# Optimization experiments

Hardware: AMD Instinct MI355X
Metric: run time of the kernel (lower is better)

## Reference

```python
import jax, jax.numpy as jnp
import numpy as np

N = 8192       # tokens (batch*seq)
D = 4096       # input_size / d_model
H = 256        # gate hidden_size
E = 64         # num_experts
K = 2          # top_k


def setup_inputs() -> dict:
    key = jax.random.key(0)
    k0, k1, k2, k3 = jax.random.split(key, 4)
    x = jax.random.normal(k0, (N, D), dtype=jnp.float32)
    # nn.Linear default init: U(-1/sqrt(fan_in), 1/sqrt(fan_in))
    w1 = jax.random.uniform(k1, (H, D), jnp.float32, -1.0, 1.0) / np.sqrt(D)
    b1 = jax.random.uniform(k2, (H,), jnp.float32, -1.0, 1.0) / np.sqrt(D)
    w2 = jax.random.uniform(k3, (E, H), jnp.float32, -1.0, 1.0) / np.sqrt(H)
    return {"x": x, "w1": w1, "b1": b1, "w2": w2}


def reference(x, w1, b1, w2):
    # MLP gate: Linear -> GELU (exact erf, torch default) -> Dropout(eval: identity) -> Linear(no bias)
    h = jax.nn.gelu(jnp.einsum('nd,hd->nh', x, w1) + b1, approximate=False)  # [N, H]
    logits = jnp.einsum('nh,eh->ne', h, w2)                                  # [N, E]
    probs = jax.nn.softmax(logits, axis=-1)                                  # [N, E]
    # deterministic top-k path (sample_topk=0 / eval mode)
    top_k_gates, top_k_indices = jax.lax.top_k(probs, K)                     # [N, K] each
    return top_k_indices, top_k_gates, probs
```

## Files before the change

kernel.cpp:

```cpp
#include <hip/hip_runtime.h>
#include <hip/hip_bf16.h>
#include <math.h>

#define NTOK 8192
#define DIN  4096
#define HG   256
#define NE   64
#define SPLITK 4
#define KSTEPS 32
#define TR   16

typedef __attribute__((ext_vector_type(8))) short short8;
typedef __attribute__((ext_vector_type(4))) short short4v;
typedef __attribute__((ext_vector_type(4))) float f32x4;

__device__ __forceinline__ unsigned short f2bf_rne(float f) {
    union { float f; unsigned int u; } v; v.f = f;
    unsigned int r = v.u + 0x7fffu + ((v.u >> 16) & 1u);
    return (unsigned short)(r >> 16);
}
__device__ __forceinline__ float bf2f(unsigned short b) {
    union { unsigned int u; float f; } v; v.u = ((unsigned int)b) << 16;
    return v.f;
}

typedef const __attribute__((address_space(1))) unsigned int* gptr_t;
typedef __attribute__((address_space(3))) unsigned int* lptr_t;
__device__ __forceinline__ void gload_lds16(const void* g, void* l) {
    __builtin_amdgcn_global_load_lds((gptr_t)g, (lptr_t)l, 16, 0, 0);
}

__global__ __launch_bounds__(512) void convert_w1_kernel(
    const float* __restrict__ w1, unsigned short* __restrict__ w1t)
{
    const int id    = blockIdx.x * 512 + threadIdx.x;
    const int lane  = id & 63;
    const int cg    = id >> 6;
    const int kstep = cg >> 5;
    const int c     = cg & 31;
    const int hl    = c >> 4;
    const int unit  = c & 15;
    const int n     = unit * 16 + (lane & 15);
    const int k     = kstep * 32 + ((lane >> 4) & 3) * 8;

    const float* src = w1 + (size_t)n * DIN + k;
    short8 v;
#pragma unroll
    for (int j = 0; j < 8; ++j) {
        float f = src[j];
        unsigned short hi = f2bf_rne(f);
        v[j] = (hl == 0) ? (short)hi : (short)f2bf_rne(f - bf2f(hi));
    }
    *(short8*)(w1t + (size_t)cg * 512 + lane * 8) = v;
}

__global__ __launch_bounds__(512, 4) void gemm1_mfma_kernel(
    const float* __restrict__ x, const unsigned short* __restrict__ w1t,
    float* __restrict__ P)
{
    __shared__ unsigned short As[2][4][512];
    __shared__ unsigned short Bs[2][2][16][512];

    const int bid  = blockIdx.x;
    const int mblk = bid & 127;
    const int s    = bid >> 7;
    const int t    = threadIdx.x;
    const int lane = t & 63;
    const int w    = t >> 6;
    const int wm   = w >> 2;
    const int wn   = w & 3;

    const int m_base = mblk * 64;
    const int kstep0 = s * KSTEPS;

    const int a_unit = t >> 7;
    const int a_slot = (t >> 1) & 63;
    const int a_half = t & 1;
    const int a_row  = a_unit * 16 + (a_slot & 15);
    const int a_koff = (a_slot >> 4) * 8 + a_half * 4;
    const float* asrc = x + (size_t)(m_base + a_row) * DIN
                          + (size_t)kstep0 * 32 + a_koff;
    const int a_ldso = a_slot * 8 + a_half * 4;

    f32x4 acc[2][4];
#pragma unroll
    for (int i = 0; i < 2; ++i)
#pragma unroll
        for (int j = 0; j < 4; ++j) acc[i][j] = (f32x4)0.f;

#define CVT4_STORE(F)                                                         \
    {   short4v vh_, vl_;                                                     \
        float ff_[4] = { (F).x, (F).y, (F).z, (F).w };                        \
        _Pragma("unroll")                                                     \
        for (int j_ = 0; j_ < 4; ++j_) {                                      \
            unsigned short h_ = f2bf_rne(ff_[j_]);                            \
            vh_[j_] = (short)h_;                                              \
            vl_[j_] = (short)f2bf_rne(ff_[j_] - bf2f(h_));                    \
        }                                                                     \
        *(short4v*)&As[0][a_unit][a_ldso] = vh_;                              \
        *(short4v*)&As[1][a_unit][a_ldso] = vl_;                              \
    }

#pragma unroll
    for (int i = 0; i < 4; ++i) {
        const int c = w * 4 + i;
        gload_lds16(w1t + ((size_t)kstep0 * 32 + c) * 512 + lane * 8,
                    &Bs[0][c >> 4][c & 15][0]);
    }
    {
        float4 a0 = *(const float4*)(asrc);
        CVT4_STORE(a0)
    }
    __syncthreads();

#pragma unroll 1
    for (int tt = 0; tt < KSTEPS; ++tt) {
        const int bcur = tt & 1, bnxt = bcur ^ 1;
        const bool last = (tt == KSTEPS - 1);

        float4 nx;
        if (!last) {
            nx = *(const float4*)(asrc + (size_t)(tt + 1) * 32);
#pragma unroll
            for (int i = 0; i < 4; ++i) {
                const int c = w * 4 + i;
                gload_lds16(w1t + ((size_t)(kstep0 + tt + 1) * 32 + c) * 512 + lane * 8,
                            &Bs[bnxt][c >> 4][c & 15][0]);
            }
        }

        short8 ahf[2], alf[2], bhf[4], blf[4];
#pragma unroll
        for (int mr = 0; mr < 2; ++mr) {
            ahf[mr] = *(const short8*)&As[0][wm * 2 + mr][lane * 8];
            alf[mr] = *(const short8*)&As[1][wm * 2 + mr][lane * 8];
        }
#pragma unroll
        for (int nr = 0; nr < 4; ++nr) {
            bhf[nr] = *(const short8*)&Bs[bcur][0][wn * 4 + nr][lane * 8];
            blf[nr] = *(const short8*)&Bs[bcur][1][wn * 4 + nr][lane * 8];
        }

#pragma unroll
        for (int mr = 0; mr < 2; ++mr)
#pragma unroll
            for (int nr = 0; nr < 4; ++nr)
                acc[mr][nr] = __builtin_amdgcn_mfma_f32_16x16x32_bf16(
                    ahf[mr], bhf[nr], acc[mr][nr], 0, 0, 0);
#pragma unroll
        for (int mr = 0; mr < 2; ++mr)
#pragma unroll
            for (int nr = 0; nr < 4; ++nr)
                acc[mr][nr] = __builtin_amdgcn_mfma_f32_16x16x32_bf16(
                    ahf[mr], blf[nr], acc[mr][nr], 0, 0, 0);
#pragma unroll
        for (int mr = 0; mr < 2; ++mr)
#pragma unroll
            for (int nr = 0; nr < 4; ++nr)
                acc[mr][nr] = __builtin_amdgcn_mfma_f32_16x16x32_bf16(
                    alf[mr], bhf[nr], acc[mr][nr], 0, 0, 0);

        if (!last) {
            __syncthreads();
            CVT4_STORE(nx)
            __syncthreads();
        }
    }
#undef CVT4_STORE

    float* pb = P + (size_t)s * ((size_t)NTOK * HG);
#pragma unroll
    for (int mr = 0; mr < 2; ++mr)
#pragma unroll
        for (int nr = 0; nr < 4; ++nr) {
            const int n = wn * 64 + nr * 16 + (lane & 15);
#pragma unroll
            for (int r = 0; r < 4; ++r) {
                const int m = m_base + wm * 32 + mr * 16 + ((lane >> 4) & 3) * 4 + r;
                pb[(size_t)m * HG + n] = acc[mr][nr][r];
            }
        }
}

__global__ __launch_bounds__(512, 4) void reduce_gate_kernel(
    const float* __restrict__ P, const float* __restrict__ b1,
    const float* __restrict__ w2, float* __restrict__ out)
{
    __shared__ float h_lds[TR][260];
    __shared__ float lg[NE][33];

    const int t    = threadIdx.x;
    const int lane = t & 63;
    const int w    = t >> 6;
    const int r0   = blockIdx.x * TR;
    const size_t SS = (size_t)NTOK * HG;

    {
        const int row = t >> 5;
        const int sg  = t & 31;
        const size_t base = (size_t)(r0 + row) * HG + sg * 8;

        float q[8];
#pragma unroll
        for (int half = 0; half < 2; ++half) {
            float4 v0 = *(const float4*)(P + base + half * 4);
            float4 v1 = *(const float4*)(P + base + SS + half * 4);
            float4 v2 = *(const float4*)(P + base + 2 * SS + half * 4);
            float4 v3 = *(const float4*)(P + base + 3 * SS + half * 4);
            float4 bb = *(const float4*)(b1 + sg * 8 + half * 4);
            q[half * 4 + 0] = v0.x + v1.x + v2.x + v3.x + bb.x;
            q[half * 4 + 1] = v0.y + v1.y + v2.y + v3.y + bb.y;
            q[half * 4 + 2] = v0.z + v1.z + v2.z + v3.z + bb.z;
            q[half * 4 + 3] = v0.w + v1.w + v2.w + v3.w + bb.w;
        }
#pragma unroll
        for (int c = 0; c < 8; ++c)
            q[c] = 0.5f * q[c] * (1.0f + erff(q[c] * 0.70710678118654752440f));

        *(float4*)&h_lds[row][sg * 8]     = make_float4(q[0], q[1], q[2], q[3]);
        *(float4*)&h_lds[row][sg * 8 + 4] = make_float4(q[4], q[5], q[6], q[7]);
    }
    __syncthreads();

    const int e0   = w * 8;
    const int rowp = lane & 15;
    const int kq   = lane >> 4;

    float acc[8];
#pragma unroll
    for (int i = 0; i < 8; ++i) acc[i] = 0.f;

    const float* w2b = w2 + (size_t)e0 * HG + kq * 64;
#pragma unroll 1
    for (int kc = 0; kc < 64; kc += 8) {
        float a[8];
        *(float4*)&a[0] = *(const float4*)&h_lds[rowp][kq * 64 + kc];
        *(float4*)&a[4] = *(const float4*)&h_lds[rowp][kq * 64 + kc + 4];
#pragma unroll
        for (int n = 0; n < 8; ++n) {
            const float* wr = w2b + (size_t)n * HG + kc;
            float4 w0 = *(const float4*)(wr);
            float4 w1v = *(const float4*)(wr + 4);
            acc[n] = fmaf(w0.x, a[0], acc[n]);
            acc[n] = fmaf(w0.y, a[1], acc[n]);
            acc[n] = fmaf(w0.z, a[2], acc[n]);
            acc[n] = fmaf(w0.w, a[3], acc[n]);
            acc[n] = fmaf(w1v.x, a[4], acc[n]);
            acc[n] = fmaf(w1v.y, a[5], acc[n]);
            acc[n] = fmaf(w1v.z, a[6], acc[n]);
            acc[n] = fmaf(w1v.w, a[7], acc[n]);
        }
    }
#pragma unroll
    for (int n = 0; n < 8; ++n) {
        acc[n] += __shfl_xor(acc[n], 16);
        acc[n] += __shfl_xor(acc[n], 32);
    }
    if (lane < 16) {
#pragma unroll
        for (int n = 0; n < 8; ++n) lg[e0 + n][rowp] = acc[n];
    }
    __syncthreads();

    if (t < TR) {
        float l[NE];
#pragma unroll
        for (int e = 0; e < NE; ++e) l[e] = lg[e][t];

        float mx = l[0];
#pragma unroll
        for (int e = 1; e < NE; ++e) mx = fmaxf(mx, l[e]);

        float ssum = 0.f;
#pragma unroll
        for (int e = 0; e < NE; ++e) { float p = expf(l[e] - mx); l[e] = p; ssum += p; }
        const float inv = 1.0f / ssum;
#pragma unroll
        for (int e = 0; e < NE; ++e) l[e] *= inv;

        float v1 = -1.0f, v2 = -2.0f;
        int   i1 = 0,     i2 = 0;
#pragma unroll
        for (int e = 0; e < NE; ++e) {
            const float p  = l[e];
            const bool  g1 = p > v1;
            const bool  g2 = p > v2;
            const float nv2 = g1 ? v1 : (g2 ? p : v2);
            const int   ni2 = g1 ? i1 : (g2 ? e : i2);
            v1 = g1 ? p : v1;
            i1 = g1 ? e : i1;
            v2 = nv2;
            i2 = ni2;
        }

        const int row = r0 + t;
        float* out_idx  = out;
        float* out_gate = out + 2 * NTOK;
        float* out_prob = out + 4 * NTOK;
        out_idx[2 * row + 0]  = (float)i1;
        out_idx[2 * row + 1]  = (float)i2;
        out_gate[2 * row + 0] = v1;
        out_gate[2 * row + 1] = v2;

        float* pr = out_prob + (size_t)row * NE;
#pragma unroll
        for (int e = 0; e < NE; e += 4)
            *(float4*)(pr + e) = make_float4(l[e], l[e + 1], l[e + 2], l[e + 3]);
    }
}

extern "C" void kernel_launch(void* const* d_in, const int* in_sizes, int n_in,
                              void* d_out, int out_size, void* d_ws, size_t ws_size,
                              hipStream_t stream) {
    const float* x  = (const float*)d_in[0];
    const float* w1 = (const float*)d_in[1];
    const float* b1 = (const float*)d_in[2];
    const float* w2 = (const float*)d_in[3];
    float* out = (float*)d_out;

    unsigned short* w1t = (unsigned short*)d_ws;
    float* P = (float*)((char*)d_ws + (4u << 20));

    convert_w1_kernel<<<512, 512, 0, stream>>>(w1, w1t);
    gemm1_mfma_kernel<<<512, 512, 0, stream>>>(x, w1t, P);
    reduce_gate_kernel<<<512, 512, 0, stream>>>(P, b1, w2, out);
}
```

Measured before the change: 91.14 us.

## Use 4-wave blocks with 64x64 warp tiles and double-buffered A in LDS

The GEMM1 kernel moves from 8 waves to 4 waves per block, so each wave computes a 64x64 output tile (4x4 MFMA tiles) instead of 32x64. This raises register reuse of the A and B fragments and cuts LDS reads per MFMA. The converted A tile is now double-buffered in LDS, which removes one of the two barriers per k-step. In exchange each wave holds more accumulator registers and fewer waves are resident to hide latency.

```diff
diff --git a/kernel.cpp b/kernel.cpp
--- a/kernel.cpp
+++ b/kernel.cpp
@@ -54,11 +54,11 @@
     *(short8*)(w1t + (size_t)cg * 512 + lane * 8) = v;
 }
 
-__global__ __launch_bounds__(512, 4) void gemm1_mfma_kernel(
+__global__ __launch_bounds__(256, 2) void gemm1_mfma_kernel(
     const float* __restrict__ x, const unsigned short* __restrict__ w1t,
     float* __restrict__ P)
 {
-    __shared__ unsigned short As[2][4][512];
+    __shared__ unsigned short As[2][2][4][512];
     __shared__ unsigned short Bs[2][2][16][512];
 
     const int bid  = blockIdx.x;
@@ -67,49 +67,48 @@
     const int t    = threadIdx.x;
     const int lane = t & 63;
     const int w    = t >> 6;
-    const int wm   = w >> 2;
-    const int wn   = w & 3;
 
     const int m_base = mblk * 64;
     const int kstep0 = s * KSTEPS;
 
-    const int a_unit = t >> 7;
-    const int a_slot = (t >> 1) & 63;
-    const int a_half = t & 1;
-    const int a_row  = a_unit * 16 + (a_slot & 15);
-    const int a_koff = (a_slot >> 4) * 8 + a_half * 4;
+    const int a_unit = t >> 6;
+    const int a_q    = t & 63;
+    const int a_row  = a_unit * 16 + (a_q & 15);
+    const int a_koff = (a_q >> 4) * 8;
     const float* asrc = x + (size_t)(m_base + a_row) * DIN
                           + (size_t)kstep0 * 32 + a_koff;
-    const int a_ldso = a_slot * 8 + a_half * 4;
-
-    f32x4 acc[2][4];
-#pragma unroll
-    for (int i = 0; i < 2; ++i)
+    const int a_ldso = a_q * 8;
+
+    f32x4 acc[4][4];
+#pragma unroll
+    for (int i = 0; i < 4; ++i)
 #pragma unroll
         for (int j = 0; j < 4; ++j) acc[i][j] = (f32x4)0.f;
 
-#define CVT4_STORE(F)                                                         \
-    {   short4v vh_, vl_;                                                     \
-        float ff_[4] = { (F).x, (F).y, (F).z, (F).w };                        \
+#define CVT8_STORE(BUF, F0, F1)                                               \
+    {   short8 vh_, vl_;                                                      \
+        float ff_[8] = { (F0).x, (F0).y, (F0).z, (F0).w,                      \
+                         (F1).x, (F1).y, (F1).z, (F1).w };                    \
         _Pragma("unroll")                                                     \
-        for (int j_ = 0; j_ < 4; ++j_) {                                      \
+        for (int j_ = 0; j_ < 8; ++j_) {                                      \
             unsigned short h_ = f2bf_rne(ff_[j_]);                            \
             vh_[j_] = (short)h_;                                              \
             vl_[j_] = (short)f2bf_rne(ff_[j_] - bf2f(h_));                    \
         }                                                                     \
-        *(short4v*)&As[0][a_unit][a_ldso] = vh_;                              \
-        *(short4v*)&As[1][a_unit][a_ldso] = vl_;                              \
-    }
-
-#pragma unroll
-    for (int i = 0; i < 4; ++i) {
-        const int c = w * 4 + i;
+        *(short8*)&As[BUF][0][a_unit][a_ldso] = vh_;                          \
+        *(short8*)&As[BUF][1][a_unit][a_ldso] = vl_;                          \
+    }
+
+#pragma unroll
+    for (int i = 0; i < 8; ++i) {
+        const int c = w * 8 + i;
         gload_lds16(w1t + ((size_t)kstep0 * 32 + c) * 512 + lane * 8,
                     &Bs[0][c >> 4][c & 15][0]);
     }
     {
         float4 a0 = *(const float4*)(asrc);
-        CVT4_STORE(a0)
+        float4 a1 = *(const float4*)(asrc + 4);
+        CVT8_STORE(0, a0, a1)
     }
     __syncthreads();
 
@@ -118,65 +117,66 @@
         const int bcur = tt & 1, bnxt = bcur ^ 1;
         const bool last = (tt == KSTEPS - 1);
 
-        float4 nx;
+        float4 nx0, nx1;
         if (!last) {
-            nx = *(const float4*)(asrc + (size_t)(tt + 1) * 32);
-#pragma unroll
-            for (int i = 0; i < 4; ++i) {
-                const int c = w * 4 + i;
+            const float* ap = asrc + (size_t)(tt + 1) * 32;
+            nx0 = *(const float4*)(ap);
+            nx1 = *(const float4*)(ap + 4);
+#pragma unroll
+            for (int i = 0; i < 8; ++i) {
+                const int c = w * 8 + i;
                 gload_lds16(w1t + ((size_t)(kstep0 + tt + 1) * 32 + c) * 512 + lane * 8,
                             &Bs[bnxt][c >> 4][c & 15][0]);
             }
         }
 
-        short8 ahf[2], alf[2], bhf[4], blf[4];
-#pragma unroll
-        for (int mr = 0; mr < 2; ++mr) {
-            ahf[mr] = *(const short8*)&As[0][wm * 2 + mr][lane * 8];
-            alf[mr] = *(const short8*)&As[1][wm * 2 + mr][lane * 8];
+        short8 ahf[4], alf[4], bhf[4], blf[4];
+#pragma unroll
+        for (int mr = 0; mr < 4; ++mr) {
+            ahf[mr] = *(const short8*)&As[bcur][0][mr][lane * 8];
+            alf[mr] = *(const short8*)&As[bcur][1][mr][lane * 8];
         }
 #pragma unroll
         for (int nr = 0; nr < 4; ++nr) {
-            bhf[nr] = *(const short8*)&Bs[bcur][0][wn * 4 + nr][lane * 8];
-            blf[nr] = *(const short8*)&Bs[bcur][1][wn * 4 + nr][lane * 8];
-        }
-
-#pragma unroll
-        for (int mr = 0; mr < 2; ++mr)
+            bhf[nr] = *(const short8*)&Bs[bcur][0][w * 4 + nr][lane * 8];
+            blf[nr] = *(const short8*)&Bs[bcur][1][w * 4 + nr][lane * 8];
+        }
+
+#pragma unroll
+        for (int mr = 0; mr < 4; ++mr)
 #pragma unroll
             for (int nr = 0; nr < 4; ++nr)
                 acc[mr][nr] = __builtin_amdgcn_mfma_f32_16x16x32_bf16(
                     ahf[mr], bhf[nr], acc[mr][nr], 0, 0, 0);
 #pragma unroll
-        for (int mr = 0; mr < 2; ++mr)
+        for (int mr = 0; mr < 4; ++mr)
 #pragma unroll
             for (int nr = 0; nr < 4; ++nr)
                 acc[mr][nr] = __builtin_amdgcn_mfma_f32_16x16x32_bf16(
                     ahf[mr], blf[nr], acc[mr][nr], 0, 0, 0);
 #pragma unroll
-        for (int mr = 0; mr < 2; ++mr)
+        for (int mr = 0; mr < 4; ++mr)
 #pragma unroll
             for (int nr = 0; nr < 4; ++nr)
                 acc[mr][nr] = __builtin_amdgcn_mfma_f32_16x16x32_bf16(
                     alf[mr], bhf[nr], acc[mr][nr], 0, 0, 0);
 
         if (!last) {
+            CVT8_STORE(bnxt, nx0, nx1)
             __syncthreads();
-            CVT4_STORE(nx)
-            __syncthreads();
-        }
-    }
-#undef CVT4_STORE
+        }
+    }
+#undef CVT8_STORE
 
     float* pb = P + (size_t)s * ((size_t)NTOK * HG);
 #pragma unroll
-    for (int mr = 0; mr < 2; ++mr)
+    for (int mr = 0; mr < 4; ++mr)
 #pragma unroll
         for (int nr = 0; nr < 4; ++nr) {
-            const int n = wn * 64 + nr * 16 + (lane & 15);
+            const int n = w * 64 + nr * 16 + (lane & 15);
 #pragma unroll
             for (int r = 0; r < 4; ++r) {
-                const int m = m_base + wm * 32 + mr * 16 + ((lane >> 4) & 3) * 4 + r;
+                const int m = m_base + mr * 16 + ((lane >> 4) & 3) * 4 + r;
                 pb[(size_t)m * HG + n] = acc[mr][nr][r];
             }
         }
@@ -322,6 +322,6 @@
     float* P = (float*)((char*)d_ws + (4u << 20));
 
     convert_w1_kernel<<<512, 512, 0, stream>>>(w1, w1t);
-    gemm1_mfma_kernel<<<512, 512, 0, stream>>>(x, w1t, P);
+    gemm1_mfma_kernel<<<512, 256, 0, stream>>>(x, w1t, P);
     reduce_gate_kernel<<<512, 512, 0, stream>>>(P, b1, w2, out);
 }
```

After: 91.77 us. Within noise of the previous version (+0.7%).

## Load GEMM1 operands directly from global into registers, dropping LDS staging

Applied to the files above, without the earlier changes.

The first GEMM kernel no longer stages x and w1 tiles through shared memory with double buffering and barriers. Each wave now loads its own A rows and pre-converted B fragments straight from global memory into registers and converts x to split bf16 per wave. This removes LDS traffic and the two barriers per k-step. In exchange, x rows are loaded and converted redundantly by the four waves sharing an M slice, B fragments are fetched by both M waves, and there is no explicit prefetch to hide global latency.

```diff
diff --git a/kernel.cpp b/kernel.cpp
--- a/kernel.cpp
+++ b/kernel.cpp
@@ -11,7 +11,6 @@
 #define TR   16
 
 typedef __attribute__((ext_vector_type(8))) short short8;
-typedef __attribute__((ext_vector_type(4))) short short4v;
 typedef __attribute__((ext_vector_type(4))) float f32x4;
 
 __device__ __forceinline__ unsigned short f2bf_rne(float f) {
@@ -22,12 +21,6 @@
 __device__ __forceinline__ float bf2f(unsigned short b) {
     union { unsigned int u; float f; } v; v.u = ((unsigned int)b) << 16;
     return v.f;
-}
-
-typedef const __attribute__((address_space(1))) unsigned int* gptr_t;
-typedef __attribute__((address_space(3))) unsigned int* lptr_t;
-__device__ __forceinline__ void gload_lds16(const void* g, void* l) {
-    __builtin_amdgcn_global_load_lds((gptr_t)g, (lptr_t)l, 16, 0, 0);
 }
 
 __global__ __launch_bounds__(512) void convert_w1_kernel(
@@ -58,9 +51,6 @@
     const float* __restrict__ x, const unsigned short* __restrict__ w1t,
     float* __restrict__ P)
 {
-    __shared__ unsigned short As[2][4][512];
-    __shared__ unsigned short Bs[2][2][16][512];
-
     const int bid  = blockIdx.x;
     const int mblk = bid & 127;
     const int s    = bid >> 7;
@@ -73,72 +63,50 @@
     const int m_base = mblk * 64;
     const int kstep0 = s * KSTEPS;
 
-    const int a_unit = t >> 7;
-    const int a_slot = (t >> 1) & 63;
-    const int a_half = t & 1;
-    const int a_row  = a_unit * 16 + (a_slot & 15);
-    const int a_koff = (a_slot >> 4) * 8 + a_half * 4;
-    const float* asrc = x + (size_t)(m_base + a_row) * DIN
-                          + (size_t)kstep0 * 32 + a_koff;
-    const int a_ldso = a_slot * 8 + a_half * 4;
+    const float* a0 = x + (size_t)(m_base + wm * 32 + (lane & 15)) * DIN
+                        + (size_t)kstep0 * 32 + ((lane >> 4) * 8);
+    const float* a1 = a0 + 16 * DIN;
+
+    const unsigned short* bbase = w1t + ((size_t)kstep0 * 32) * 512 + lane * 8;
 
     f32x4 acc[2][4];
 #pragma unroll
     for (int i = 0; i < 2; ++i)
 #pragma unroll
         for (int j = 0; j < 4; ++j) acc[i][j] = (f32x4)0.f;
-
-#define CVT4_STORE(F)                                                         \
-    {   short4v vh_, vl_;                                                     \
-        float ff_[4] = { (F).x, (F).y, (F).z, (F).w };                        \
-        _Pragma("unroll")                                                     \
-        for (int j_ = 0; j_ < 4; ++j_) {                                      \
-            unsigned short h_ = f2bf_rne(ff_[j_]);                            \
-            vh_[j_] = (short)h_;                                              \
-            vl_[j_] = (short)f2bf_rne(ff_[j_] - bf2f(h_));                    \
-        }                                                                     \
-        *(short4v*)&As[0][a_unit][a_ldso] = vh_;                              \
-        *(short4v*)&As[1][a_unit][a_ldso] = vl_;                              \
-    }
-
-#pragma unroll
-    for (int i = 0; i < 4; ++i) {
-        const int c = w * 4 + i;
-        gload_lds16(w1t + ((size_t)kstep0 * 32 + c) * 512 + lane * 8,
-                    &Bs[0][c >> 4][c & 15][0]);
-    }
-    {
-        float4 a0 = *(const float4*)(asrc);
-        CVT4_STORE(a0)
-    }
-    __syncthreads();
 
 #pragma unroll 1
     for (int tt = 0; tt < KSTEPS; ++tt) {
-        const int bcur = tt & 1, bnxt = bcur ^ 1;
-        const bool last = (tt == KSTEPS - 1);
-
-        float4 nx;
-        if (!last) {
-            nx = *(const float4*)(asrc + (size_t)(tt + 1) * 32);
-#pragma unroll
-            for (int i = 0; i < 4; ++i) {
-                const int c = w * 4 + i;
-                gload_lds16(w1t + ((size_t)(kstep0 + tt + 1) * 32 + c) * 512 + lane * 8,
-                            &Bs[bnxt][c >> 4][c & 15][0]);
+        const float* ap0 = a0 + (size_t)tt * 32;
+        const float* ap1 = a1 + (size_t)tt * 32;
+        float4 f00 = *(const float4*)(ap0);
+        float4 f01 = *(const float4*)(ap0 + 4);
+        float4 f10 = *(const float4*)(ap1);
+        float4 f11 = *(const float4*)(ap1 + 4);
+
+        const unsigned short* bk = bbase + (size_t)tt * 32 * 512;
+        short8 bh[4], bl[4];
+#pragma unroll
+        for (int nr = 0; nr < 4; ++nr) {
+            bh[nr] = *(const short8*)(bk + (wn * 4 + nr) * 512);
+            bl[nr] = *(const short8*)(bk + (16 + wn * 4 + nr) * 512);
+        }
+
+        short8 ah[2], al[2];
+        {
+            float ff0[8] = { f00.x, f00.y, f00.z, f00.w,
+                             f01.x, f01.y, f01.z, f01.w };
+            float ff1[8] = { f10.x, f10.y, f10.z, f10.w,
+                             f11.x, f11.y, f11.z, f11.w };
+#pragma unroll
+            for (int j = 0; j < 8; ++j) {
+                unsigned short h0 = f2bf_rne(ff0[j]);
+                ah[0][j] = (short)h0;
+                al[0][j] = (short)f2bf_rne(ff0[j] - bf2f(h0));
+                unsigned short h1 = f2bf_rne(ff1[j]);
+                ah[1][j] = (short)h1;
+                al[1][j] = (short)f2bf_rne(ff1[j] - bf2f(h1));
             }
-        }
-
-        short8 ahf[2], alf[2], bhf[4], blf[4];
-#pragma unroll
-        for (int mr = 0; mr < 2; ++mr) {
-            ahf[mr] = *(const short8*)&As[0][wm * 2 + mr][lane * 8];
-            alf[mr] = *(const short8*)&As[1][wm * 2 + mr][lane * 8];
-        }
-#pragma unroll
-        for (int nr = 0; nr < 4; ++nr) {
-            bhf[nr] = *(const short8*)&Bs[bcur][0][wn * 4 + nr][lane * 8];
-            blf[nr] = *(const short8*)&Bs[bcur][1][wn * 4 + nr][lane * 8];
         }
 
 #pragma unroll
@@ -146,27 +114,20 @@
 #pragma unroll
             for (int nr = 0; nr < 4; ++nr)
                 acc[mr][nr] = __builtin_amdgcn_mfma_f32_16x16x32_bf16(
-                    ahf[mr], bhf[nr], acc[mr][nr], 0, 0, 0);
+                    ah[mr], bh[nr], acc[mr][nr], 0, 0, 0);
 #pragma unroll
         for (int mr = 0; mr < 2; ++mr)
 #pragma unroll
             for (int nr = 0; nr < 4; ++nr)
                 acc[mr][nr] = __builtin_amdgcn_mfma_f32_16x16x32_bf16(
-                    ahf[mr], blf[nr], acc[mr][nr], 0, 0, 0);
+                    ah[mr], bl[nr], acc[mr][nr], 0, 0, 0);
 #pragma unroll
         for (int mr = 0; mr < 2; ++mr)
 #pragma unroll
             for (int nr = 0; nr < 4; ++nr)
                 acc[mr][nr] = __builtin_amdgcn_mfma_f32_16x16x32_bf16(
-                    alf[mr], bhf[nr], acc[mr][nr], 0, 0, 0);
-
-        if (!last) {
-            __syncthreads();
-            CVT4_STORE(nx)
-            __syncthreads();
-        }
-    }
-#undef CVT4_STORE
+                    al[mr], bh[nr], acc[mr][nr], 0, 0, 0);
+    }
 
     float* pb = P + (size_t)s * ((size_t)NTOK * HG);
 #pragma unroll
```

New measurement: 127.5 us. +39.9%, slower.

## Split GEMM1 N dimension across two blocks and hand-tune waits and barriers

Applied to the files above, without the earlier changes.

Each GEMM1 block now computes half of the 256 hidden columns, so the grid doubles to 1024 blocks and the B tile in LDS halves. Launch bounds rise to 8 blocks per CU. __syncthreads is replaced with explicit vmcnt/lgkmcnt waits plus s_barrier, and s_setprio is raised around the MFMA section. The A-tile load mapping changes to row-contiguous float4 reads. Together these aim at more occupancy and more overlap of loads with math. The cost is that every block converts the x tile to bf16 hi/lo again, so x traffic and conversion work double.

```diff
diff --git a/kernel.cpp b/kernel.cpp
--- a/kernel.cpp
+++ b/kernel.cpp
@@ -29,6 +29,11 @@
 __device__ __forceinline__ void gload_lds16(const void* g, void* l) {
     __builtin_amdgcn_global_load_lds((gptr_t)g, (lptr_t)l, 16, 0, 0);
 }
+
+#define WAIT_VMCNT0 { asm volatile("s_waitcnt vmcnt(0)" ::: "memory"); \
+                      __builtin_amdgcn_sched_barrier(0); }
+#define WAIT_LGKM0  { asm volatile("s_waitcnt lgkmcnt(0)" ::: "memory"); \
+                      __builtin_amdgcn_sched_barrier(0); }
 
 __global__ __launch_bounds__(512) void convert_w1_kernel(
     const float* __restrict__ w1, unsigned short* __restrict__ w1t)
@@ -54,16 +59,17 @@
     *(short8*)(w1t + (size_t)cg * 512 + lane * 8) = v;
 }
 
-__global__ __launch_bounds__(512, 4) void gemm1_mfma_kernel(
+__global__ __launch_bounds__(512, 8) void gemm1_mfma_kernel(
     const float* __restrict__ x, const unsigned short* __restrict__ w1t,
     float* __restrict__ P)
 {
     __shared__ unsigned short As[2][4][512];
-    __shared__ unsigned short Bs[2][2][16][512];
+    __shared__ unsigned short Bs[2][2][8][512];
 
     const int bid  = blockIdx.x;
     const int mblk = bid & 127;
-    const int s    = bid >> 7;
+    const int nt   = (bid >> 7) & 1;
+    const int s    = bid >> 8;
     const int t    = threadIdx.x;
     const int lane = t & 63;
     const int w    = t >> 6;
@@ -73,20 +79,18 @@
     const int m_base = mblk * 64;
     const int kstep0 = s * KSTEPS;
 
-    const int a_unit = t >> 7;
-    const int a_slot = (t >> 1) & 63;
-    const int a_half = t & 1;
-    const int a_row  = a_unit * 16 + (a_slot & 15);
-    const int a_koff = (a_slot >> 4) * 8 + a_half * 4;
+    const int a_row   = t >> 3;
+    const int a_k4    = (t & 7) * 4;
+    const int a_unit  = a_row >> 4;
+    const int a_off   = (((a_k4 >> 3) << 4) | (a_row & 15)) * 8 + (a_k4 & 7);
     const float* asrc = x + (size_t)(m_base + a_row) * DIN
-                          + (size_t)kstep0 * 32 + a_koff;
-    const int a_ldso = a_slot * 8 + a_half * 4;
-
-    f32x4 acc[2][4];
+                          + (size_t)kstep0 * 32 + a_k4;
+
+    f32x4 acc[2][2];
 #pragma unroll
     for (int i = 0; i < 2; ++i)
 #pragma unroll
-        for (int j = 0; j < 4; ++j) acc[i][j] = (f32x4)0.f;
+        for (int j = 0; j < 2; ++j) acc[i][j] = (f32x4)0.f;
 
 #define CVT4_STORE(F)                                                         \
     {   short4v vh_, vl_;                                                     \
@@ -97,83 +101,89 @@
             vh_[j_] = (short)h_;                                              \
             vl_[j_] = (short)f2bf_rne(ff_[j_] - bf2f(h_));                    \
         }                                                                     \
-        *(short4v*)&As[0][a_unit][a_ldso] = vh_;                              \
-        *(short4v*)&As[1][a_unit][a_ldso] = vl_;                              \
-    }
-
-#pragma unroll
-    for (int i = 0; i < 4; ++i) {
-        const int c = w * 4 + i;
-        gload_lds16(w1t + ((size_t)kstep0 * 32 + c) * 512 + lane * 8,
-                    &Bs[0][c >> 4][c & 15][0]);
-    }
+        *(short4v*)&As[0][a_unit][a_off] = vh_;                               \
+        *(short4v*)&As[1][a_unit][a_off] = vl_;                               \
+    }
+
+#define ISSUE_B(KS, BUF)                                                      \
+    _Pragma("unroll")                                                         \
+    for (int i_ = 0; i_ < 2; ++i_) {                                          \
+        const int c_  = w * 2 + i_;                                           \
+        const int hl_ = c_ >> 3, un_ = c_ & 7;                                \
+        gload_lds16(w1t + ((size_t)(KS) * 32 + hl_ * 16 + nt * 8 + un_) * 512 \
+                        + lane * 8,                                           \
+                    &Bs[BUF][hl_][un_][0]);                                   \
+    }
+
     {
         float4 a0 = *(const float4*)(asrc);
+        ISSUE_B(kstep0, 0)
         CVT4_STORE(a0)
-    }
-    __syncthreads();
+        WAIT_VMCNT0
+        WAIT_LGKM0
+        __builtin_amdgcn_s_barrier();
+    }
+
+    int cur = 0;
 
 #pragma unroll 1
     for (int tt = 0; tt < KSTEPS; ++tt) {
-        const int bcur = tt & 1, bnxt = bcur ^ 1;
-        const bool last = (tt == KSTEPS - 1);
+        const bool has1 = (tt + 1 < KSTEPS);
 
         float4 nx;
-        if (!last) {
+        if (has1) {
             nx = *(const float4*)(asrc + (size_t)(tt + 1) * 32);
-#pragma unroll
-            for (int i = 0; i < 4; ++i) {
-                const int c = w * 4 + i;
-                gload_lds16(w1t + ((size_t)(kstep0 + tt + 1) * 32 + c) * 512 + lane * 8,
-                            &Bs[bnxt][c >> 4][c & 15][0]);
-            }
-        }
-
-        short8 ahf[2], alf[2], bhf[4], blf[4];
+            ISSUE_B(kstep0 + tt + 1, cur ^ 1)
+        }
+
+        short8 ahf[2], alf[2];
 #pragma unroll
         for (int mr = 0; mr < 2; ++mr) {
             ahf[mr] = *(const short8*)&As[0][wm * 2 + mr][lane * 8];
             alf[mr] = *(const short8*)&As[1][wm * 2 + mr][lane * 8];
         }
-#pragma unroll
-        for (int nr = 0; nr < 4; ++nr) {
-            bhf[nr] = *(const short8*)&Bs[bcur][0][wn * 4 + nr][lane * 8];
-            blf[nr] = *(const short8*)&Bs[bcur][1][wn * 4 + nr][lane * 8];
-        }
-
-#pragma unroll
-        for (int mr = 0; mr < 2; ++mr)
-#pragma unroll
-            for (int nr = 0; nr < 4; ++nr)
+
+        __builtin_amdgcn_s_setprio(1);
+#pragma unroll
+        for (int nr = 0; nr < 2; ++nr) {
+            short8 bh = *(const short8*)&Bs[cur][0][wn * 2 + nr][lane * 8];
+            short8 bl = *(const short8*)&Bs[cur][1][wn * 2 + nr][lane * 8];
+#pragma unroll
+            for (int mr = 0; mr < 2; ++mr)
                 acc[mr][nr] = __builtin_amdgcn_mfma_f32_16x16x32_bf16(
-                    ahf[mr], bhf[nr], acc[mr][nr], 0, 0, 0);
-#pragma unroll
-        for (int mr = 0; mr < 2; ++mr)
-#pragma unroll
-            for (int nr = 0; nr < 4; ++nr)
+                    ahf[mr], bh, acc[mr][nr], 0, 0, 0);
+#pragma unroll
+            for (int mr = 0; mr < 2; ++mr)
                 acc[mr][nr] = __builtin_amdgcn_mfma_f32_16x16x32_bf16(
-                    ahf[mr], blf[nr], acc[mr][nr], 0, 0, 0);
-#pragma unroll
-        for (int mr = 0; mr < 2; ++mr)
-#pragma unroll
-            for (int nr = 0; nr < 4; ++nr)
+                    ahf[mr], bl, acc[mr][nr], 0, 0, 0);
+#pragma unroll
+            for (int mr = 0; mr < 2; ++mr)
                 acc[mr][nr] = __builtin_amdgcn_mfma_f32_16x16x32_bf16(
-                    alf[mr], bhf[nr], acc[mr][nr], 0, 0, 0);
-
-        if (!last) {
-            __syncthreads();
+                    alf[mr], bh, acc[mr][nr], 0, 0, 0);
+        }
+        __builtin_amdgcn_s_setprio(0);
+
+        if (has1) {
+            WAIT_LGKM0
+            __builtin_amdgcn_s_barrier();
+
             CVT4_STORE(nx)
-            __syncthreads();
-        }
-    }
+
+            WAIT_VMCNT0
+            WAIT_LGKM0
+            __builtin_amdgcn_s_barrier();
+            cur ^= 1;
+        }
+    }
+#undef ISSUE_B
 #undef CVT4_STORE
 
     float* pb = P + (size_t)s * ((size_t)NTOK * HG);
 #pragma unroll
     for (int mr = 0; mr < 2; ++mr)
 #pragma unroll
-        for (int nr = 0; nr < 4; ++nr) {
-            const int n = wn * 64 + nr * 16 + (lane & 15);
+        for (int nr = 0; nr < 2; ++nr) {
+            const int n = nt * 128 + wn * 32 + nr * 16 + (lane & 15);
 #pragma unroll
             for (int r = 0; r < 4; ++r) {
                 const int m = m_base + wm * 32 + mr * 16 + ((lane >> 4) & 3) * 4 + r;
@@ -322,6 +332,6 @@
     float* P = (float*)((char*)d_ws + (4u << 20));
 
     convert_w1_kernel<<<512, 512, 0, stream>>>(w1, w1t);
-    gemm1_mfma_kernel<<<512, 512, 0, stream>>>(x, w1t, P);
+    gemm1_mfma_kernel<<<1024, 512, 0, stream>>>(x, w1t, P);
     reduce_gate_kernel<<<512, 512, 0, stream>>>(P, b1, w2, out);
 }
```

New measurement: 97.19 us. 1.07x slower.
